# Optimization experiments

Measured on AMD Instinct MI355X. Metric: run time of the kernel, lower is better.

Reference implementation:

```python
import jax, jax.numpy as jnp
import numpy as np

VOCAB, EMB_DIM, HIDDEN, NUM_CLASSES = 100000, 128, 256, 20
B, S = 4096, 200


def setup_inputs() -> dict:
    key = jax.random.key(0)
    k1, k2, k3, k4, k5, k6, k7 = jax.random.split(key, 7)
    x = jax.random.randint(k1, (B, S), 0, VOCAB, dtype=jnp.int64)
    seq_lengths = jnp.maximum(jax.random.randint(k2, (B,), 0, S, dtype=jnp.int64), 1)
    emb = jax.random.normal(k3, (VOCAB, EMB_DIM), dtype=jnp.float32) * 0.02
    emb = emb.at[0].set(0.0)  # padding_idx=0
    W1 = jax.random.normal(k4, (EMB_DIM, HIDDEN), dtype=jnp.float32) * (1.0 / np.sqrt(EMB_DIM))
    b1 = jax.random.normal(k5, (HIDDEN,), dtype=jnp.float32) * 0.01
    W2 = jax.random.normal(k6, (HIDDEN, NUM_CLASSES), dtype=jnp.float32) * (1.0 / np.sqrt(HIDDEN))
    b2 = jax.random.normal(k7, (NUM_CLASSES,), dtype=jnp.float32) * 0.01
    return {"x": x, "seq_lengths": seq_lengths, "emb": emb, "W1": W1, "b1": b1, "W2": W2, "b2": b2}


def reference(x, seq_lengths, emb, W1, b1, W2, b2):
    # Embedding lookup: [B, S, D]
    e = emb[x]
    # Masked mean over first seq_lengths[i] positions (fused, no per-sample loop)
    mask = (jnp.arange(S)[None, :] < seq_lengths[:, None]).astype(e.dtype)  # [B, S]
    pooled = jnp.einsum('bsd,bs->bd', e, mask) / seq_lengths[:, None].astype(e.dtype)
    # MLP (dropout is identity in eval mode)
    hidden = jax.nn.relu(pooled @ W1 + b1)
    return hidden @ W2 + b2
```

## Files before the change

kernel.cpp:

```cpp
#include <hip/hip_runtime.h>
#include <hip/hip_bf16.h>

#define B 4096
#define S 200
#define SPAD 224
#define EMB_DIM 128
#define HIDDEN 256
#define NUM_CLASSES 20

__global__ __launch_bounds__(256) void pool_kernel(
    const int* __restrict__ x,
    const int* __restrict__ lens,
    const float* __restrict__ emb,
    float* __restrict__ pooled)
{
    const int b = blockIdx.x;
    const int t = threadIdx.x;
    const int L = lens[b];

    __shared__ int sidx[SPAD];
    __shared__ float4 tmp[8][32];

    if (t < SPAD) {
        int v = 0;
        if (t < L) v = x[(long)b * S + t];
        sidx[t] = v;
    }
    __syncthreads();

    const int g = t >> 5;
    const int d = t & 31;

    float4 a0 = make_float4(0.f, 0.f, 0.f, 0.f);
    float4 a1 = a0, a2 = a0, a3 = a0;

    const int Lpad = (L + 31) & ~31;
    for (int base = g; base < Lpad; base += 32) {
        const int i0 = sidx[base];
        const int i1 = sidx[base + 8];
        const int i2 = sidx[base + 16];
        const int i3 = sidx[base + 24];
        const float4 v0 = ((const float4*)(emb + (long)i0 * EMB_DIM))[d];
        const float4 v1 = ((const float4*)(emb + (long)i1 * EMB_DIM))[d];
        const float4 v2 = ((const float4*)(emb + (long)i2 * EMB_DIM))[d];
        const float4 v3 = ((const float4*)(emb + (long)i3 * EMB_DIM))[d];
        a0.x += v0.x; a0.y += v0.y; a0.z += v0.z; a0.w += v0.w;
        a1.x += v1.x; a1.y += v1.y; a1.z += v1.z; a1.w += v1.w;
        a2.x += v2.x; a2.y += v2.y; a2.z += v2.z; a2.w += v2.w;
        a3.x += v3.x; a3.y += v3.y; a3.z += v3.z; a3.w += v3.w;
    }
    a0.x += a1.x + a2.x + a3.x;
    a0.y += a1.y + a2.y + a3.y;
    a0.z += a1.z + a2.z + a3.z;
    a0.w += a1.w + a2.w + a3.w;

    tmp[g][d] = a0;
    __syncthreads();

    if (t < 32) {
        float4 s0 = tmp[0][t];
        #pragma unroll
        for (int gg = 1; gg < 8; ++gg) {
            const float4 v = tmp[gg][t];
            s0.x += v.x; s0.y += v.y; s0.z += v.z; s0.w += v.w;
        }
        const float inv = 1.0f / (float)L;
        s0.x *= inv; s0.y *= inv; s0.z *= inv; s0.w *= inv;
        ((float4*)(pooled + (long)b * EMB_DIM))[t] = s0;
    }
}

#define TB 8
__global__ __launch_bounds__(256) void mlp_kernel(
    const float* __restrict__ pooled,
    const float* __restrict__ W1,
    const float* __restrict__ b1,
    const float* __restrict__ W2,
    const float* __restrict__ b2,
    float* __restrict__ out)
{
    __shared__ float P[TB][EMB_DIM];
    __shared__ float H[TB][HIDDEN];

    const int t = threadIdx.x;
    const int b0 = blockIdx.x * TB;

    for (int i = t; i < TB * EMB_DIM; i += 256) {
        P[i >> 7][i & 127] = pooled[(long)b0 * EMB_DIM + i];
    }
    __syncthreads();

    float acc[TB];
    #pragma unroll
    for (int r = 0; r < TB; ++r) acc[r] = 0.f;

    for (int k4 = 0; k4 < EMB_DIM; k4 += 4) {
        float4 p[TB];
        #pragma unroll
        for (int r = 0; r < TB; ++r) p[r] = *(const float4*)&P[r][k4];
        #pragma unroll
        for (int kk = 0; kk < 4; ++kk) {
            const float w = W1[(k4 + kk) * HIDDEN + t];
            #pragma unroll
            for (int r = 0; r < TB; ++r) {
                const float pv = (kk == 0) ? p[r].x : (kk == 1) ? p[r].y
                               : (kk == 2) ? p[r].z : p[r].w;
                acc[r] += pv * w;
            }
        }
    }

    const float bb = b1[t];
    #pragma unroll
    for (int r = 0; r < TB; ++r) H[r][t] = fmaxf(acc[r] + bb, 0.f);
    __syncthreads();

    if (t < TB * NUM_CLASSES) {
        const int r = t / NUM_CLASSES;
        const int c = t - r * NUM_CLASSES;
        float a = b2[c];
        for (int k = 0; k < HIDDEN; ++k) {
            a += H[r][k] * W2[k * NUM_CLASSES + c];
        }
        out[(long)(b0 + r) * NUM_CLASSES + c] = a;
    }
}

extern "C" void kernel_launch(void* const* d_in, const int* in_sizes, int n_in,
                              void* d_out, int out_size, void* d_ws, size_t ws_size,
                              hipStream_t stream) {
    const int*   x    = (const int*)d_in[0];
    const int*   lens = (const int*)d_in[1];
    const float* emb  = (const float*)d_in[2];
    const float* W1   = (const float*)d_in[3];
    const float* b1   = (const float*)d_in[4];
    const float* W2   = (const float*)d_in[5];
    const float* b2   = (const float*)d_in[6];
    float*       out  = (float*)d_out;

    float* pooled = (float*)d_ws;

    pool_kernel<<<B, 256, 0, stream>>>(x, lens, emb, pooled);
    mlp_kernel<<<B / TB, 256, 0, stream>>>(pooled, W1, b1, W2, b2, out);
}
```

Measured before the change: 135.6 us.

## Convert embedding table to bf16 dim-sliced layout and gather per slice

Each call now converts the fp32 embedding table to bf16 in a layout split into 8 dimension slices of 16 values. Pooling blocks then each handle one slice for 8 rows, so the slice they touch stays small enough to be reused from cache across rows. Gathered bytes are halved but the table is reconverted on every call, and bf16 rounding adds precision loss. The second MLP layer also splits its dot product into two accumulators.

New measurement: 137.5 us. No clear change (+1.4%).

```diff
diff --git a/kernel.cpp b/kernel.cpp
--- a/kernel.cpp
+++ b/kernel.cpp
@@ -3,70 +3,107 @@
 
 #define B 4096
 #define S 200
-#define SPAD 224
 #define EMB_DIM 128
 #define HIDDEN 256
 #define NUM_CLASSES 20
+#define VOCAB 100000
+#define NSLICE 8
+#define SDIM 16
+#define SP 224
 
-__global__ __launch_bounds__(256) void pool_kernel(
+typedef __attribute__((ext_vector_type(8))) unsigned short ushort8;
+
+__device__ __forceinline__ unsigned short f2bf(float f) {
+    unsigned u = __float_as_uint(f);
+    unsigned r = u + 0x7fffu + ((u >> 16) & 1u);
+    return (unsigned short)(r >> 16);
+}
+
+__global__ __launch_bounds__(256) void convert_kernel(
+    const float* __restrict__ emb,
+    unsigned short* __restrict__ embh)
+{
+    const int t = threadIdx.x;
+    const int v = blockIdx.x * 16 + (t >> 4);
+    const int d = t & 15;
+    const float4 a = *(const float4*)(emb + (long)v * EMB_DIM + d * 8);
+    const float4 b = *(const float4*)(emb + (long)v * EMB_DIM + d * 8 + 4);
+    ushort8 o;
+    o[0] = f2bf(a.x); o[1] = f2bf(a.y); o[2] = f2bf(a.z); o[3] = f2bf(a.w);
+    o[4] = f2bf(b.x); o[5] = f2bf(b.y); o[6] = f2bf(b.z); o[7] = f2bf(b.w);
+    const int s = d >> 1, h = d & 1;
+    *(ushort8*)(embh + (long)s * VOCAB * SDIM + (long)v * SDIM + h * 8) = o;
+}
+
+__global__ __launch_bounds__(256) void gather_kernel(
     const int* __restrict__ x,
     const int* __restrict__ lens,
-    const float* __restrict__ emb,
+    const unsigned short* __restrict__ embh,
     float* __restrict__ pooled)
 {
-    const int b = blockIdx.x;
-    const int t = threadIdx.x;
-    const int L = lens[b];
+    __shared__ int sidx[8][SP];
+    __shared__ int sL[8];
 
-    __shared__ int sidx[SPAD];
-    __shared__ float4 tmp[8][32];
+    const int t  = threadIdx.x;
+    const int s  = blockIdx.x & 7;
+    const int rg = blockIdx.x >> 3;
+    const unsigned short* embS = embh + (long)s * VOCAB * SDIM;
 
-    if (t < SPAD) {
-        int v = 0;
-        if (t < L) v = x[(long)b * S + t];
-        sidx[t] = v;
+    {
+        const int r   = t >> 5;
+        const int p0  = t & 31;
+        const int row = rg * 8 + r;
+        const int L   = lens[row];
+        if (p0 == 0) sL[r] = L;
+        for (int p = p0; p < SP; p += 32)
+            sidx[r][p] = (p < L) ? x[(long)row * S + p] : 0;
     }
     __syncthreads();
 
-    const int g = t >> 5;
-    const int d = t & 31;
+    const int w  = t >> 6;
+    const int l  = t & 63;
+    const int pl = l >> 1;
+    const int h  = l & 1;
 
-    float4 a0 = make_float4(0.f, 0.f, 0.f, 0.f);
-    float4 a1 = a0, a2 = a0, a3 = a0;
+    #pragma unroll
+    for (int rr = 0; rr < 2; ++rr) {
+        const int r2 = 2 * w + rr;
+        const int L2 = sL[r2];
+        const int nR = (L2 + 31) >> 5;
 
-    const int Lpad = (L + 31) & ~31;
-    for (int base = g; base < Lpad; base += 32) {
-        const int i0 = sidx[base];
-        const int i1 = sidx[base + 8];
-        const int i2 = sidx[base + 16];
-        const int i3 = sidx[base + 24];
-        const float4 v0 = ((const float4*)(emb + (long)i0 * EMB_DIM))[d];
-        const float4 v1 = ((const float4*)(emb + (long)i1 * EMB_DIM))[d];
-        const float4 v2 = ((const float4*)(emb + (long)i2 * EMB_DIM))[d];
-        const float4 v3 = ((const float4*)(emb + (long)i3 * EMB_DIM))[d];
-        a0.x += v0.x; a0.y += v0.y; a0.z += v0.z; a0.w += v0.w;
-        a1.x += v1.x; a1.y += v1.y; a1.z += v1.z; a1.w += v1.w;
-        a2.x += v2.x; a2.y += v2.y; a2.z += v2.z; a2.w += v2.w;
-        a3.x += v3.x; a3.y += v3.y; a3.z += v3.z; a3.w += v3.w;
-    }
-    a0.x += a1.x + a2.x + a3.x;
-    a0.y += a1.y + a2.y + a3.y;
-    a0.z += a1.z + a2.z + a3.z;
-    a0.w += a1.w + a2.w + a3.w;
+        float acc[8];
+        #pragma unroll
+        for (int f = 0; f < 8; ++f) acc[f] = 0.f;
 
-    tmp[g][d] = a0;
-    __syncthreads();
+        int cur = sidx[r2][pl];
+        for (int it = 0; it < nR; ++it) {
+            const uint4 q = *(const uint4*)(embS + (long)cur * SDIM + h * 8);
+            const int nxt = (it + 1 < nR) ? sidx[r2][pl + ((it + 1) << 5)] : 0;
+            acc[0] += __uint_as_float(q.x << 16);
+            acc[1] += __uint_as_float(q.x & 0xffff0000u);
+            acc[2] += __uint_as_float(q.y << 16);
+            acc[3] += __uint_as_float(q.y & 0xffff0000u);
+            acc[4] += __uint_as_float(q.z << 16);
+            acc[5] += __uint_as_float(q.z & 0xffff0000u);
+            acc[6] += __uint_as_float(q.w << 16);
+            acc[7] += __uint_as_float(q.w & 0xffff0000u);
+            cur = nxt;
+        }
 
-    if (t < 32) {
-        float4 s0 = tmp[0][t];
         #pragma unroll
-        for (int gg = 1; gg < 8; ++gg) {
-            const float4 v = tmp[gg][t];
-            s0.x += v.x; s0.y += v.y; s0.z += v.z; s0.w += v.w;
+        for (int st = 2; st <= 32; st <<= 1) {
+            #pragma unroll
+            for (int f = 0; f < 8; ++f) acc[f] += __shfl_xor(acc[f], st, 64);
         }
-        const float inv = 1.0f / (float)L;
-        s0.x *= inv; s0.y *= inv; s0.z *= inv; s0.w *= inv;
-        ((float4*)(pooled + (long)b * EMB_DIM))[t] = s0;
+
+        if (l < 2) {
+            const float invL = 1.0f / (float)L2;
+            float* dst = pooled + (long)(rg * 8 + r2) * EMB_DIM + s * SDIM + h * 8;
+            *(float4*)dst       = make_float4(acc[0] * invL, acc[1] * invL,
+                                              acc[2] * invL, acc[3] * invL);
+            *(float4*)(dst + 4) = make_float4(acc[4] * invL, acc[5] * invL,
+                                              acc[6] * invL, acc[7] * invL);
+        }
     }
 }
 
@@ -85,9 +122,8 @@
     const int t = threadIdx.x;
     const int b0 = blockIdx.x * TB;
 
-    for (int i = t; i < TB * EMB_DIM; i += 256) {
+    for (int i = t; i < TB * EMB_DIM; i += 256)
         P[i >> 7][i & 127] = pooled[(long)b0 * EMB_DIM + i];
-    }
     __syncthreads();
 
     float acc[TB];
@@ -118,11 +154,12 @@
     if (t < TB * NUM_CLASSES) {
         const int r = t / NUM_CLASSES;
         const int c = t - r * NUM_CLASSES;
-        float a = b2[c];
-        for (int k = 0; k < HIDDEN; ++k) {
-            a += H[r][k] * W2[k * NUM_CLASSES + c];
+        float a0 = 0.f, a1 = 0.f;
+        for (int k = 0; k < HIDDEN; k += 2) {
+            a0 += H[r][k]     * W2[(k)     * NUM_CLASSES + c];
+            a1 += H[r][k + 1] * W2[(k + 1) * NUM_CLASSES + c];
         }
-        out[(long)(b0 + r) * NUM_CLASSES + c] = a;
+        out[(long)(b0 + r) * NUM_CLASSES + c] = a0 + a1 + b2[c];
     }
 }
 
@@ -138,8 +175,10 @@
     const float* b2   = (const float*)d_in[6];
     float*       out  = (float*)d_out;
 
-    float* pooled = (float*)d_ws;
+    unsigned short* embh  = (unsigned short*)d_ws;
+    float* pooled = (float*)((char*)d_ws + (long)VOCAB * EMB_DIM * 2);
 
-    pool_kernel<<<B, 256, 0, stream>>>(x, lens, emb, pooled);
+    convert_kernel<<<VOCAB / 16, 256, 0, stream>>>(emb, embh);
+    gather_kernel<<<(B / 8) * NSLICE, 256, 0, stream>>>(x, lens, embh, pooled);
     mlp_kernel<<<B / TB, 256, 0, stream>>>(pooled, W1, b1, W2, b2, out);
 }
```
